# Kernel tuning notes

Measured on AMD Instinct MI355X. Metric: run time of the kernel, lower is better.

The kernel has to match this reference:

```python
import jax, jax.numpy as jnp
import numpy as np

B, S, HID = 4, 512, 768
NH, HD = 12, 64          # num_heads, head_size = HID // NH
REL = 64                 # rel_dim
NEG_INF = -1e9


def setup_inputs() -> dict:
    key = jax.random.key(0)
    ks = jax.random.split(key, 12)
    input_tensor = jax.random.normal(ks[0], (B, S, HID), jnp.float32)
    graph_matrix = (jax.random.uniform(ks[1], (B, S, S)) < 0.3).astype(jnp.float32)
    # end_mask: one-hot at the last position (null attention slot)
    end_mask = jnp.zeros((B, S), jnp.float32).at[:, S - 1].set(1.0)
    rel_embeddings = jax.random.normal(ks[2], (B, S, S, REL), jnp.float32)
    w = lambda k, shp: jax.random.normal(k, shp, jnp.float32) * 0.02
    return {
        "input_tensor": input_tensor,
        "graph_matrix": graph_matrix,
        "end_mask": end_mask,
        "rel_embeddings": rel_embeddings,
        "Wq": w(ks[3], (HID, HID)), "bq": jnp.zeros((HID,), jnp.float32),
        "Wk": w(ks[4], (HID, HID)), "bk": jnp.zeros((HID,), jnp.float32),
        "Wv": w(ks[5], (HID, HID)), "bv": jnp.zeros((HID,), jnp.float32),
        "Wr": w(ks[6], (REL, HD)), "br": jnp.zeros((HD,), jnp.float32),
    }


def reference(input_tensor, graph_matrix, end_mask, rel_embeddings,
              Wq, bq, Wk, bk, Wv, bv, Wr, br):
    # use_null_att_pos: allow attending to the end/null slot
    g = graph_matrix + end_mask[:, None, :]              # (B,S,S)
    neg_inf_mask = (1.0 - g) * NEG_INF                   # (B,S,S)

    def heads(x):  # (B,S,HID) -> (B,NH,S,HD)
        return x.reshape(B, S, NH, HD).transpose(0, 2, 1, 3)

    q = heads(input_tensor @ Wq + bq)
    k = heads(input_tensor @ Wk + bk)
    v = heads(input_tensor @ Wv + bv)

    rel = rel_embeddings @ Wr + br                       # (B,S,S,HD), shared over heads
    # matmul_rel: (x_i * (y_j + z_ij)).sum(-1) = q.k^T + q.rel, per head
    scores = (jnp.einsum('bhid,bhjd->bhij', q, k)
              + jnp.einsum('bhid,bijd->bhij', q, rel))   # (B,NH,S,S)
    scores = scores / jnp.sqrt(jnp.float32(HD)) + neg_inf_mask[:, None]
    probs = jax.nn.softmax(scores, axis=-1)              # dropout p=0 -> identity

    ctx = jnp.einsum('bhij,bhjd->bhid', probs, v)        # (B,NH,S,HD)
    return ctx.transpose(0, 2, 1, 3).reshape(B, S, NH * HD)
```

## Files before the change

kernel.cpp:

```cpp
#include <hip/hip_runtime.h>
#include <hip/hip_bf16.h>
#include <cstddef>
#include <cstdint>

typedef __attribute__((ext_vector_type(8))) short bf16x8;
typedef __attribute__((ext_vector_type(4))) float f32x4;

#define MFMA16(a, b, c) __builtin_amdgcn_mfma_f32_16x16x32_bf16((a), (b), (c), 0, 0, 0)

static constexpr int B = 4, S = 512, HID = 768, NH = 12, HD = 64;
static constexpr int QKV_N = B * NH * S * HD;
static constexpr size_t SCORES_N = (size_t)B * NH * S * S;

__device__ __forceinline__ short f2bf(float f) {
  unsigned u = __builtin_bit_cast(unsigned, f);
  u += 0x7FFFu + ((u >> 16) & 1u);
  return (short)(u >> 16);
}
__device__ __forceinline__ float bf2f(short s) {
  unsigned u = ((unsigned)(unsigned short)s) << 16;
  return __builtin_bit_cast(float, u);
}
__device__ __forceinline__ bf16x8 ld_cvt8(const float* __restrict__ p) {
  float4 a = *reinterpret_cast<const float4*>(p);
  float4 b = *reinterpret_cast<const float4*>(p + 4);
  bf16x8 r;
  r[0] = f2bf(a.x); r[1] = f2bf(a.y); r[2] = f2bf(a.z); r[3] = f2bf(a.w);
  r[4] = f2bf(b.x); r[5] = f2bf(b.y); r[6] = f2bf(b.z); r[7] = f2bf(b.w);
  return r;
}

__global__ __launch_bounds__(256) void k_qkv(
    const float* __restrict__ x,
    const float* __restrict__ Wq, const float* __restrict__ bq,
    const float* __restrict__ Wk, const float* __restrict__ bk,
    const float* __restrict__ Wv, const float* __restrict__ bv,
    short* __restrict__ qkv) {
  __shared__ short As[64 * 40];
  __shared__ short Bs[64 * 40];
  const int m0 = blockIdx.x * 64;
  const int nt = blockIdx.y;
  const int mat = nt / 12;
  const int nc0 = (nt % 12) * 64;
  const float* __restrict__ W    = (mat == 0) ? Wq : (mat == 1) ? Wk : Wv;
  const float* __restrict__ bias = (mat == 0) ? bq : (mat == 1) ? bk : bv;
  short* __restrict__ outp = qkv + (size_t)mat * QKV_N;
  const int t = threadIdx.x;
  const int w = t >> 6, lane = t & 63;
  const int wm = (w >> 1) * 32, wn = (w & 1) * 32;
  const int lr = lane & 15, lk = lane >> 4;
  f32x4 acc[2][2] = {};
  for (int kk = 0; kk < 768; kk += 32) {
#pragma unroll
    for (int it = 0; it < 2; ++it) {
      int f = it * 256 + t;
      {
        int r = f >> 3, c4 = f & 7;
        float4 v = *reinterpret_cast<const float4*>(x + (size_t)(m0 + r) * 768 + kk + c4 * 4);
        short* d = &As[r * 40 + c4 * 4];
        d[0] = f2bf(v.x); d[1] = f2bf(v.y); d[2] = f2bf(v.z); d[3] = f2bf(v.w);
      }
      {
        int kr = f >> 4, c4 = f & 15;
        float4 v = *reinterpret_cast<const float4*>(W + (size_t)(kk + kr) * 768 + nc0 + c4 * 4);
        int c = c4 * 4;
        Bs[(c + 0) * 40 + kr] = f2bf(v.x);
        Bs[(c + 1) * 40 + kr] = f2bf(v.y);
        Bs[(c + 2) * 40 + kr] = f2bf(v.z);
        Bs[(c + 3) * 40 + kr] = f2bf(v.w);
      }
    }
    __syncthreads();
    bf16x8 a0 = *reinterpret_cast<const bf16x8*>(&As[(wm + lr) * 40 + lk * 8]);
    bf16x8 a1 = *reinterpret_cast<const bf16x8*>(&As[(wm + 16 + lr) * 40 + lk * 8]);
    bf16x8 b0 = *reinterpret_cast<const bf16x8*>(&Bs[(wn + lr) * 40 + lk * 8]);
    bf16x8 b1 = *reinterpret_cast<const bf16x8*>(&Bs[(wn + 16 + lr) * 40 + lk * 8]);
    acc[0][0] = MFMA16(a0, b0, acc[0][0]);
    acc[0][1] = MFMA16(a0, b1, acc[0][1]);
    acc[1][0] = MFMA16(a1, b0, acc[1][0]);
    acc[1][1] = MFMA16(a1, b1, acc[1][1]);
    __syncthreads();
  }
#pragma unroll
  for (int mf = 0; mf < 2; ++mf)
#pragma unroll
    for (int nf = 0; nf < 2; ++nf) {
      int col = nc0 + wn + nf * 16 + lr;
      float bv_ = bias[col];
      int h = col >> 6, d = col & 63;
#pragma unroll
      for (int reg = 0; reg < 4; ++reg) {
        int m = m0 + wm + mf * 16 + lk * 4 + reg;
        int b_ = m >> 9, i = m & 511;
        outp[(size_t)((b_ * NH + h) * S + i) * HD + d] = f2bf(acc[mf][nf][reg] + bv_);
      }
    }
}

__global__ __launch_bounds__(256) void k_qr(const short* __restrict__ q,
                                            const float* __restrict__ Wr,
                                            short* __restrict__ qr) {
  const int i0 = blockIdx.x * 64;
  const int h = blockIdx.y, b = blockIdx.z;
  const short* __restrict__ qp = q + (size_t)((b * NH + h) * S) * HD;
  short* __restrict__ op = qr + (size_t)((b * NH + h) * S) * HD;
  const int t = threadIdx.x;
  const int w = t >> 6, lane = t & 63;
  const int wm = (w >> 1) * 32, wn = (w & 1) * 32;
  const int lr = lane & 15, lk = lane >> 4;
  f32x4 acc[2][2] = {};
#pragma unroll
  for (int ks = 0; ks < 2; ++ks) {
    int k0 = ks * 32 + lk * 8;
    bf16x8 a0 = *reinterpret_cast<const bf16x8*>(qp + (size_t)(i0 + wm + lr) * 64 + k0);
    bf16x8 a1 = *reinterpret_cast<const bf16x8*>(qp + (size_t)(i0 + wm + 16 + lr) * 64 + k0);
    bf16x8 b0 = ld_cvt8(Wr + (size_t)(wn + lr) * 64 + k0);
    bf16x8 b1 = ld_cvt8(Wr + (size_t)(wn + 16 + lr) * 64 + k0);
    acc[0][0] = MFMA16(a0, b0, acc[0][0]);
    acc[0][1] = MFMA16(a0, b1, acc[0][1]);
    acc[1][0] = MFMA16(a1, b0, acc[1][0]);
    acc[1][1] = MFMA16(a1, b1, acc[1][1]);
  }
#pragma unroll
  for (int mf = 0; mf < 2; ++mf)
#pragma unroll
    for (int nf = 0; nf < 2; ++nf) {
      int r = wn + nf * 16 + lr;
#pragma unroll
      for (int reg = 0; reg < 4; ++reg) {
        int i = i0 + wm + mf * 16 + lk * 4 + reg;
        op[(size_t)i * 64 + r] = f2bf(acc[mf][nf][reg] * 0.125f);
      }
    }
}

__global__ __launch_bounds__(256) void k_qk(const short* __restrict__ q,
                                            const short* __restrict__ kmat,
                                            const float* __restrict__ graph,
                                            const float* __restrict__ endm,
                                            float* __restrict__ scores) {
  const int j0 = blockIdx.x * 64, i0 = blockIdx.y * 64;
  const int bh = blockIdx.z;
  const int b = bh / NH;
  const short* __restrict__ qp = q + (size_t)(bh * S) * HD;
  const short* __restrict__ kp = kmat + (size_t)(bh * S) * HD;
  const int t = threadIdx.x;
  const int w = t >> 6, lane = t & 63;
  const int wm = (w >> 1) * 32, wn = (w & 1) * 32;
  const int lr = lane & 15, lk = lane >> 4;
  f32x4 acc[2][2] = {};
#pragma unroll
  for (int ks = 0; ks < 2; ++ks) {
    int k0 = ks * 32 + lk * 8;
    bf16x8 a0 = *reinterpret_cast<const bf16x8*>(qp + (size_t)(i0 + wm + lr) * 64 + k0);
    bf16x8 a1 = *reinterpret_cast<const bf16x8*>(qp + (size_t)(i0 + wm + 16 + lr) * 64 + k0);
    bf16x8 b0 = *reinterpret_cast<const bf16x8*>(kp + (size_t)(j0 + wn + lr) * 64 + k0);
    bf16x8 b1 = *reinterpret_cast<const bf16x8*>(kp + (size_t)(j0 + wn + 16 + lr) * 64 + k0);
    acc[0][0] = MFMA16(a0, b0, acc[0][0]);
    acc[0][1] = MFMA16(a0, b1, acc[0][1]);
    acc[1][0] = MFMA16(a1, b0, acc[1][0]);
    acc[1][1] = MFMA16(a1, b1, acc[1][1]);
  }
#pragma unroll
  for (int mf = 0; mf < 2; ++mf)
#pragma unroll
    for (int nf = 0; nf < 2; ++nf) {
      int j = j0 + wn + nf * 16 + lr;
      float e = endm[b * S + j];
#pragma unroll
      for (int reg = 0; reg < 4; ++reg) {
        int i = i0 + wm + mf * 16 + lk * 4 + reg;
        float g = graph[(size_t)(b * S + i) * S + j];
        scores[((size_t)bh * S + i) * S + j] =
            acc[mf][nf][reg] * 0.125f + (1.0f - g - e) * (-1e9f);
      }
    }
}

__global__ __launch_bounds__(256) void k_relsm(const short* __restrict__ qrb,
                                               const float* __restrict__ rel,
                                               const float* __restrict__ scores,
                                               short* __restrict__ probs) {
  __shared__ short pl[16 * 520];
  __shared__ float den_lds[64];
  const int i = blockIdx.x, b = blockIdx.y;
  const int t = threadIdx.x;
  const int w = t >> 6, lane = t & 63;
  const int lr = lane & 15, fq = lane >> 4;
  const int hA = (lr < NH) ? lr : 0;
  const short* qrow = qrb + ((size_t)(b * NH + hA) * S + i) * 64;
  bf16x8 a0 = *reinterpret_cast<const bf16x8*>(qrow + fq * 8);
  bf16x8 a1 = *reinterpret_cast<const bf16x8*>(qrow + 32 + fq * 8);
  const float* rp = rel + ((size_t)(b * S) + i) * S * 64;
  const float* sc = scores + ((size_t)(b * NH) * S + i) * S;
  float den[4] = {0.f, 0.f, 0.f, 0.f};
#pragma unroll
  for (int tt = 0; tt < 8; ++tt) {
    int j0 = w * 128 + tt * 16;
    const float* rrow = rp + (size_t)(j0 + lr) * 64 + fq * 8;
    bf16x8 b0 = ld_cvt8(rrow);
    bf16x8 b1 = ld_cvt8(rrow + 32);
    f32x4 acc = {};
    acc = MFMA16(a0, b0, acc);
    acc = MFMA16(a1, b1, acc);
#pragma unroll
    for (int r = 0; r < 4; ++r) {
      int h = fq * 4 + r;
      float s = acc[r] + sc[(size_t)h * S * S + j0 + lr];
      float pe = __expf(fminf(s, 80.0f));
      den[r] += pe;
      pl[h * 520 + j0 + lr] = f2bf(pe);
    }
  }
#pragma unroll
  for (int r = 0; r < 4; ++r) {
    float d = den[r];
    d += __shfl_xor(d, 1); d += __shfl_xor(d, 2);
    d += __shfl_xor(d, 4); d += __shfl_xor(d, 8);
    den[r] = d;
  }
  if (lr == 0) {
#pragma unroll
    for (int r = 0; r < 4; ++r) den_lds[w * 16 + fq * 4 + r] = den[r];
  }
  __syncthreads();
  const int h = t >> 4, jseg = t & 15;
  if (h < NH) {
    float inv = 1.0f / (den_lds[h] + den_lds[16 + h] + den_lds[32 + h] + den_lds[48 + h]);
    short* op = probs + ((size_t)(b * NH + h) * S + i) * S + jseg * 32;
    const short* lp = &pl[h * 520 + jseg * 32];
#pragma unroll
    for (int c = 0; c < 4; ++c) {
      bf16x8 x = *reinterpret_cast<const bf16x8*>(lp + c * 8);
      bf16x8 y;
#pragma unroll
      for (int u = 0; u < 8; ++u) y[u] = f2bf(bf2f(x[u]) * inv);
      *reinterpret_cast<bf16x8*>(op + c * 8) = y;
    }
  }
}

__global__ __launch_bounds__(256) void k_pv2(const short* __restrict__ probs,
                                             const short* __restrict__ v,
                                             float* __restrict__ out) {
  __shared__ short vt[64 * 72];
  const int i0 = blockIdx.x * 64;
  const int h = blockIdx.y, b = blockIdx.z;
  const short* __restrict__ vp = v + (size_t)((b * NH + h) * S) * HD;
  const short* __restrict__ pp = probs + (size_t)((b * NH + h) * S) * S;
  const int t = threadIdx.x;
  const int w = t >> 6, lane = t & 63;
  const int wm = (w >> 1) * 32, wn = (w & 1) * 32;
  const int lr = lane & 15, lk = lane >> 4;
  f32x4 acc[2][2] = {};
  for (int j0 = 0; j0 < S; j0 += 64) {
    __syncthreads();
#pragma unroll
    for (int it = 0; it < 2; ++it) {
      int jr = it * 32 + (t >> 3), c8 = t & 7;
      bf16x8 vv = *reinterpret_cast<const bf16x8*>(vp + (size_t)(j0 + jr) * 64 + c8 * 8);
      int jsw = (((jr >> 3) ^ c8) << 3) | (jr & 7);
#pragma unroll
      for (int u = 0; u < 8; ++u) vt[(c8 * 8 + u) * 72 + jsw] = vv[u];
    }
    __syncthreads();
#pragma unroll
    for (int ks = 0; ks < 2; ++ks) {
      const short* prow = pp + j0 + ks * 32 + lk * 8;
      bf16x8 a0 = *reinterpret_cast<const bf16x8*>(prow + (size_t)(i0 + wm + lr) * S);
      bf16x8 a1 = *reinterpret_cast<const bf16x8*>(prow + (size_t)(i0 + wm + 16 + lr) * S);
      int r0 = wn + lr, r1 = wn + 16 + lr;
      int jb = ks * 4 + lk;
      bf16x8 b0 = *reinterpret_cast<const bf16x8*>(&vt[r0 * 72 + ((jb ^ ((r0 >> 3) & 7)) << 3)]);
      bf16x8 b1 = *reinterpret_cast<const bf16x8*>(&vt[r1 * 72 + ((jb ^ ((r1 >> 3) & 7)) << 3)]);
      acc[0][0] = MFMA16(a0, b0, acc[0][0]);
      acc[0][1] = MFMA16(a0, b1, acc[0][1]);
      acc[1][0] = MFMA16(a1, b0, acc[1][0]);
      acc[1][1] = MFMA16(a1, b1, acc[1][1]);
    }
  }
#pragma unroll
  for (int mf = 0; mf < 2; ++mf)
#pragma unroll
    for (int nf = 0; nf < 2; ++nf) {
      int d = wn + nf * 16 + lr;
#pragma unroll
      for (int reg = 0; reg < 4; ++reg) {
        int i = i0 + wm + mf * 16 + lk * 4 + reg;
        out[((size_t)(b * S) + i) * HID + h * 64 + d] = acc[mf][nf][reg];
      }
    }
}

extern "C" void kernel_launch(void* const* d_in, const int* in_sizes, int n_in,
                              void* d_out, int out_size, void* d_ws, size_t ws_size,
                              hipStream_t stream) {
  const float* x     = (const float*)d_in[0];
  const float* graph = (const float*)d_in[1];
  const float* endm  = (const float*)d_in[2];
  const float* rel   = (const float*)d_in[3];
  const float* Wq = (const float*)d_in[4];  const float* bq = (const float*)d_in[5];
  const float* Wk = (const float*)d_in[6];  const float* bk = (const float*)d_in[7];
  const float* Wv = (const float*)d_in[8];  const float* bv = (const float*)d_in[9];
  const float* Wr = (const float*)d_in[10];

  short* qb  = (short*)d_ws;
  short* kb  = qb + QKV_N;
  short* vb  = kb + QKV_N;
  short* qrb = vb + QKV_N;
  float* scores = (float*)(qrb + QKV_N);
  short* probs  = (short*)(scores + SCORES_N);
  const size_t need = (size_t)4 * QKV_N * 2 + SCORES_N * 4 + SCORES_N * 2;
  if (ws_size < need) return;

  k_qkv<<<dim3(32, 36), 256, 0, stream>>>(x, Wq, bq, Wk, bk, Wv, bv, qb);
  k_qr<<<dim3(8, NH, B), 256, 0, stream>>>(qb, Wr, qrb);
  k_qk<<<dim3(8, 8, B * NH), 256, 0, stream>>>(qb, kb, graph, endm, scores);
  k_relsm<<<dim3(S, B), 256, 0, stream>>>(qrb, rel, scores, probs);
  k_pv2<<<dim3(8, NH, B), 256, 0, stream>>>(probs, vb, (float*)d_out);
}
```

Baseline: 173.3 us.

## Store masked scores as fp16 in head-interleaved layout, prefetch rel loads

The intermediate score buffer becomes fp16 instead of fp32, with the mask constant lowered to -30000 so it fits the fp16 range. The buffer is laid out (b,i,h,j) so each softmax block reads a contiguous slab. The rel-embedding loop now uses nontemporal loads with one-step register prefetch. Unnormalised probabilities stay in registers rather than an LDS staging buffer, and normalised values are written straight to global memory. This cuts score traffic and LDS use, but the probs stores become scattered 2-byte writes and the lower mask value and fp16 precision could shift numerics slightly.

```diff
diff --git a/kernel.cpp b/kernel.cpp
--- a/kernel.cpp
+++ b/kernel.cpp
@@ -1,5 +1,6 @@
 #include <hip/hip_runtime.h>
 #include <hip/hip_bf16.h>
+#include <hip/hip_fp16.h>
 #include <cstddef>
 #include <cstdint>
 
@@ -27,6 +28,15 @@
   bf16x8 r;
   r[0] = f2bf(a.x); r[1] = f2bf(a.y); r[2] = f2bf(a.z); r[3] = f2bf(a.w);
   r[4] = f2bf(b.x); r[5] = f2bf(b.y); r[6] = f2bf(b.z); r[7] = f2bf(b.w);
+  return r;
+}
+__device__ __forceinline__ f32x4 ld4nt(const float* p) {
+  return __builtin_nontemporal_load(reinterpret_cast<const f32x4*>(p));
+}
+__device__ __forceinline__ bf16x8 cvt8(f32x4 a, f32x4 b) {
+  bf16x8 r;
+  r[0] = f2bf(a[0]); r[1] = f2bf(a[1]); r[2] = f2bf(a[2]); r[3] = f2bf(a[3]);
+  r[4] = f2bf(b[0]); r[5] = f2bf(b[1]); r[6] = f2bf(b[2]); r[7] = f2bf(b[3]);
   return r;
 }
 
@@ -138,10 +148,10 @@
                                             const short* __restrict__ kmat,
                                             const float* __restrict__ graph,
                                             const float* __restrict__ endm,
-                                            float* __restrict__ scores) {
+                                            __half* __restrict__ sc) {
   const int j0 = blockIdx.x * 64, i0 = blockIdx.y * 64;
   const int bh = blockIdx.z;
-  const int b = bh / NH;
+  const int b = bh / NH, hh = bh % NH;
   const short* __restrict__ qp = q + (size_t)(bh * S) * HD;
   const short* __restrict__ kp = kmat + (size_t)(bh * S) * HD;
   const int t = threadIdx.x;
@@ -171,17 +181,16 @@
       for (int reg = 0; reg < 4; ++reg) {
         int i = i0 + wm + mf * 16 + lk * 4 + reg;
         float g = graph[(size_t)(b * S + i) * S + j];
-        scores[((size_t)bh * S + i) * S + j] =
-            acc[mf][nf][reg] * 0.125f + (1.0f - g - e) * (-1e9f);
+        float s = acc[mf][nf][reg] * 0.125f + (1.0f - g - e) * (-30000.0f);
+        sc[(((size_t)b * S + i) * NH + hh) * S + j] = __float2half(s);
       }
     }
 }
 
 __global__ __launch_bounds__(256) void k_relsm(const short* __restrict__ qrb,
                                                const float* __restrict__ rel,
-                                               const float* __restrict__ scores,
+                                               const __half* __restrict__ sc,
                                                short* __restrict__ probs) {
-  __shared__ short pl[16 * 520];
   __shared__ float den_lds[64];
   const int i = blockIdx.x, b = blockIdx.y;
   const int t = threadIdx.x;
@@ -191,26 +200,32 @@
   const short* qrow = qrb + ((size_t)(b * NH + hA) * S + i) * 64;
   bf16x8 a0 = *reinterpret_cast<const bf16x8*>(qrow + fq * 8);
   bf16x8 a1 = *reinterpret_cast<const bf16x8*>(qrow + 32 + fq * 8);
-  const float* rp = rel + ((size_t)(b * S) + i) * S * 64;
-  const float* sc = scores + ((size_t)(b * NH) * S + i) * S;
+  const float* rp = rel + (((size_t)(b * S) + i) * S + (size_t)(w * 128 + lr)) * 64 + fq * 8;
+  const __half* scp = sc + ((size_t)(b * S) + i) * NH * S;
+  float p[8][4];
   float den[4] = {0.f, 0.f, 0.f, 0.f};
+  f32x4 c0 = ld4nt(rp), c1 = ld4nt(rp + 4), c2 = ld4nt(rp + 32), c3 = ld4nt(rp + 36);
 #pragma unroll
   for (int tt = 0; tt < 8; ++tt) {
-    int j0 = w * 128 + tt * 16;
-    const float* rrow = rp + (size_t)(j0 + lr) * 64 + fq * 8;
-    bf16x8 b0 = ld_cvt8(rrow);
-    bf16x8 b1 = ld_cvt8(rrow + 32);
+    f32x4 n0, n1, n2, n3;
+    if (tt < 7) {
+      const float* rn = rp + (size_t)(tt + 1) * 1024;
+      n0 = ld4nt(rn); n1 = ld4nt(rn + 4); n2 = ld4nt(rn + 32); n3 = ld4nt(rn + 36);
+    }
+    bf16x8 b0 = cvt8(c0, c1), b1 = cvt8(c2, c3);
     f32x4 acc = {};
     acc = MFMA16(a0, b0, acc);
     acc = MFMA16(a1, b1, acc);
+    const int j0 = w * 128 + tt * 16;
 #pragma unroll
     for (int r = 0; r < 4; ++r) {
       int h = fq * 4 + r;
-      float s = acc[r] + sc[(size_t)h * S * S + j0 + lr];
+      float s = acc[r] + __half2float(scp[h * S + j0 + lr]);
       float pe = __expf(fminf(s, 80.0f));
       den[r] += pe;
-      pl[h * 520 + j0 + lr] = f2bf(pe);
-    }
+      p[tt][r] = pe;
+    }
+    if (tt < 7) { c0 = n0; c1 = n1; c2 = n2; c3 = n3; }
   }
 #pragma unroll
   for (int r = 0; r < 4; ++r) {
@@ -224,18 +239,20 @@
     for (int r = 0; r < 4; ++r) den_lds[w * 16 + fq * 4 + r] = den[r];
   }
   __syncthreads();
-  const int h = t >> 4, jseg = t & 15;
-  if (h < NH) {
-    float inv = 1.0f / (den_lds[h] + den_lds[16 + h] + den_lds[32 + h] + den_lds[48 + h]);
-    short* op = probs + ((size_t)(b * NH + h) * S + i) * S + jseg * 32;
-    const short* lp = &pl[h * 520 + jseg * 32];
-#pragma unroll
-    for (int c = 0; c < 4; ++c) {
-      bf16x8 x = *reinterpret_cast<const bf16x8*>(lp + c * 8);
-      bf16x8 y;
-#pragma unroll
-      for (int u = 0; u < 8; ++u) y[u] = f2bf(bf2f(x[u]) * inv);
-      *reinterpret_cast<bf16x8*>(op + c * 8) = y;
+  float invd[4];
+#pragma unroll
+  for (int r = 0; r < 4; ++r) {
+    int h = fq * 4 + r;
+    invd[r] = 1.0f / (den_lds[h] + den_lds[16 + h] + den_lds[32 + h] + den_lds[48 + h]);
+  }
+#pragma unroll
+  for (int tt = 0; tt < 8; ++tt) {
+    int j0 = w * 128 + tt * 16;
+#pragma unroll
+    for (int r = 0; r < 4; ++r) {
+      int h = fq * 4 + r;
+      if (h < NH)
+        probs[((size_t)(b * NH + h) * S + i) * S + j0 + lr] = f2bf(p[tt][r] * invd[r]);
     }
   }
 }
@@ -308,9 +325,9 @@
   short* kb  = qb + QKV_N;
   short* vb  = kb + QKV_N;
   short* qrb = vb + QKV_N;
-  float* scores = (float*)(qrb + QKV_N);
-  short* probs  = (short*)(scores + SCORES_N);
-  const size_t need = (size_t)4 * QKV_N * 2 + SCORES_N * 4 + SCORES_N * 2;
+  __half* scores = (__half*)(qrb + QKV_N);
+  short* probs   = (short*)(scores + SCORES_N);
+  const size_t need = (size_t)4 * QKV_N * 2 + SCORES_N * 2 + SCORES_N * 2;
   if (ws_size < need) return;
 
   k_qkv<<<dim3(32, 36), 256, 0, stream>>>(x, Wq, bq, Wk, bk, Wv, bv, qb);
```

Measured after the change: 162.4 us. 1.07x faster.
